# Kernel optimization log

Measured on AMD Instinct MI355X. Metric: run time of the kernel, lower is better.

Reference implementation:

```python
import jax, jax.numpy as jnp
import numpy as np
from jax import lax

N_VNS = 65536
N_CNS = 32768
DV = 4                      # VN degree per graph
N_EDGES = N_VNS * DV
BATCH = 64
NUM_ITER = 8
LLR_MAX = 20.0
ATANH_CLIP = 1.0 - 1e-7


def _graph(rng, n_vns, n_cns, dv):
    # edges sorted by VN (matches argsort(vn_con) in the original)
    vn = np.repeat(np.arange(n_vns, dtype=np.int32), dv)
    cn = rng.integers(0, n_cns, size=n_vns * dv).astype(np.int32)
    perm_v2c = np.argsort(cn, kind='stable').astype(np.int32)   # ind_cn
    perm_c2v = np.argsort(perm_v2c, kind='stable').astype(np.int32)  # ind_cn_inv
    return vn, cn, perm_v2c, perm_c2v


def setup_inputs() -> dict:
    rng = np.random.default_rng(0)
    vn_x, cn_x, pv_x, pc_x = _graph(rng, N_VNS, N_CNS, DV)
    vn_z, cn_z, pv_z, pc_z = _graph(rng, N_VNS, N_CNS, DV)
    key = jax.random.key(0)
    k1, k2, k3 = jax.random.split(key, 3)
    # channel LLRs for X/Y/Z errors (positive-ish, typical for low error rate)
    llr_ch = jax.random.uniform(k1, (3, N_VNS, BATCH), jnp.float32) * 10.0
    syndrome_x = jax.random.randint(k2, (N_CNS, BATCH), 0, 2, jnp.int32)
    syndrome_z = jax.random.randint(k3, (N_CNS, BATCH), 0, 2, jnp.int32)
    return {
        'llr_ch': llr_ch,
        'syndrome_x': syndrome_x,
        'syndrome_z': syndrome_z,
        'vn_ids_x': jnp.asarray(vn_x),
        'vn_ids_z': jnp.asarray(vn_z),
        'cn_ids_x': jnp.asarray(cn_x[pv_x]),   # CN id per edge, in CN-sorted order
        'cn_ids_z': jnp.asarray(cn_z[pv_z]),
        'perm_v2c_x': jnp.asarray(pv_x),
        'perm_v2c_z': jnp.asarray(pv_z),
        'perm_c2v_x': jnp.asarray(pc_x),
        'perm_c2v_z': jnp.asarray(pc_z),
        'num_iter': NUM_ITER,
    }


def _vn_update(msg_x, msg_z, llrx, llry, llrz, vn_x, vn_z, n_vns):
    # per-VN sums of incoming c2v messages (msg_* are [E, B], VN-sorted)
    sum_x = jax.ops.segment_sum(msg_x, vn_x, num_segments=n_vns)  # from H_x graph
    sum_z = jax.ops.segment_sum(msg_z, vn_z, num_segments=n_vns)  # from H_z graph
    llry_all = sum_x + sum_z + llry
    llrx_hx = sum_z + llrx
    llrz_hz = sum_x + llrz
    # extrinsic per-edge LLRs (exclude intrinsic message)
    llrz_hx = llrz_hz[vn_x] - msg_x
    llry_hx = llry_all[vn_x] - msg_x
    llrx_hz = llrx_hx[vn_z] - msg_z
    llry_hz = llry_all[vn_z] - msg_z
    # quaternary -> binary marginalization: log((1+e^-a)/(e^-b + e^-c))
    new_msg_x = jax.nn.softplus(-llrx_hx)[vn_x] - jnp.logaddexp(-llrz_hx, -llry_hx)
    new_msg_z = jax.nn.softplus(-llrz_hz)[vn_z] - jnp.logaddexp(-llrx_hz, -llry_hz)
    return new_msg_x, new_msg_z


def _cn_update_tanh(msg, cn_ids, n_cns, synd_pm):
    # msg: [E, B] in CN-sorted order; synd_pm: [C, B] in {+1,-1}
    t = jnp.tanh(msg * 0.5)
    t = jnp.where(t == 0.0, 1e-12, t)
    prod = jax.ops.segment_prod(t, cn_ids, num_segments=n_cns)  # [C, B]
    prod = prod * synd_pm
    ext = prod[cn_ids] / t                      # extrinsic product
    ext = jnp.where(jnp.abs(ext) < 1e-7, 0.0, ext)
    ext = jnp.clip(ext, -ATANH_CLIP, ATANH_CLIP)
    return 2.0 * jnp.arctanh(ext)


def reference(llr_ch, syndrome_x, syndrome_z, vn_ids_x, vn_ids_z,
              cn_ids_x, cn_ids_z, perm_v2c_x, perm_v2c_z,
              perm_c2v_x, perm_c2v_z, num_iter):
    n_vns = llr_ch.shape[1]
    n_cns_x = syndrome_x.shape[0]
    n_cns_z = syndrome_z.shape[0]
    batch = llr_ch.shape[2]
    ex = vn_ids_x.shape[0]
    ez = vn_ids_z.shape[0]
    dt = llr_ch.dtype

    llr = jnp.clip(llr_ch, -LLR_MAX, LLR_MAX)
    llrx, llry, llrz = llr[0], llr[1], llr[2]
    sx = (1.0 - 2.0 * syndrome_x).astype(dt)  # {0,1} -> {+1,-1}
    sz = (1.0 - 2.0 * syndrome_z).astype(dt)

    def step(carry, _):
        msg_x, msg_z = carry
        nmx, nmz = _vn_update(msg_x, msg_z, llrx, llry, llrz,
                              vn_ids_x, vn_ids_z, n_vns)
        nmx = jnp.clip(nmx, -LLR_MAX, LLR_MAX)
        nmz = jnp.clip(nmz, -LLR_MAX, LLR_MAX)
        # permute VN-order -> CN-order, CN update, permute back
        cx = _cn_update_tanh(nmx[perm_v2c_x], cn_ids_x, n_cns_x, sx)
        cz = _cn_update_tanh(nmz[perm_v2c_z], cn_ids_z, n_cns_z, sz)
        return (cx[perm_c2v_x], cz[perm_c2v_z]), None

    init = (jnp.zeros((ex, batch), dt), jnp.zeros((ez, batch), dt))
    (msg_x, msg_z), _ = lax.scan(step, init, None, length=num_iter)

    # final marginals (sum_only VN update)
    sum_x = jax.ops.segment_sum(msg_x, vn_ids_x, num_segments=n_vns)
    sum_z = jax.ops.segment_sum(msg_z, vn_ids_z, num_segments=n_vns)
    llrx_hx = sum_z + llrx
    llry_all = sum_x + sum_z + llry
    llrz_hz = sum_x + llrz
    return jnp.stack([llrx_hx, llry_all, llrz_hz])  # [3, N, B]
```

## Files before the change

### kernel.cpp

```cpp
#include <hip/hip_runtime.h>

#define N_VNS 65536
#define N_CNS 32768
#define DV 4
#define NE (N_VNS * DV)
#define B 64
#define BH 16
#define NQ (B / BH)
#define NITER 8

#define TANH10 0.9999999958776927

__device__ __forceinline__ double sp_(double y) {
    return fmax(y, 0.0) + log1p(exp(-fabs(y)));
}
__device__ __forceinline__ double clipllr(double x) {
    return fmin(fmax(x, -20.0), 20.0);
}

__global__ void rowptr_k(const int* __restrict__ cn_x, const int* __restrict__ cn_z,
                         int* __restrict__ sx, int* __restrict__ ex,
                         int* __restrict__ sz, int* __restrict__ ez) {
    int i = blockIdx.x * blockDim.x + threadIdx.x;
    const int* cn = blockIdx.y ? cn_z : cn_x;
    int* s = blockIdx.y ? sz : sx;
    int* e = blockIdx.y ? ez : ex;
    int c = cn[i];
    if (i == 0 || cn[i - 1] != c) s[c] = i;
    if (i == NE - 1 || cn[i + 1] != c) e[c] = i + 1;
}

template <bool FIRST>
__global__ void vn_k(const float* __restrict__ llr,
                     const double* __restrict__ mLx, const double* __restrict__ mLz,
                     double* __restrict__ tx, double* __restrict__ tz,
                     int q) {
    int tid = blockIdx.x * blockDim.x + threadIdx.x;
    int v = tid >> 4, b = tid & 15;
    long base = (long)v * (DV * BH) + b;

    double mx[DV], mz[DV], exk[DV], ezk[DV];
    double sumx = 0.0, sumz = 0.0;
#pragma unroll
    for (int k = 0; k < DV; ++k) {
        if (FIRST) { mx[k] = 0.0; mz[k] = 0.0; exk[k] = 0.0; ezk[k] = 0.0; }
        else {
            mx[k] = mLx[base + k * BH];  exk[k] = tx[base + k * BH];
            mz[k] = mLz[base + k * BH];  ezk[k] = tz[base + k * BH];
        }
        sumx += mx[k]; sumz += mz[k];
    }
    long li = (long)v * B + q * BH + b;
    double lx = clipllr((double)llr[li]);
    double ly = clipllr((double)llr[(long)N_VNS * B + li]);
    double lz = clipllr((double)llr[2L * N_VNS * B + li]);

    double llrx_hx  = sumz + lx;
    double llry_all = sumx + sumz + ly;
    double llrz_hz  = sumx + lz;

    double dX = fabs(llrz_hz - llry_all);
    double cX = sp_(-llrx_hx) + fmin(llrz_hz, llry_all) - log1p(exp(-dX));
    double tCX = tanh(0.5 * cX);
    double dZ = fabs(llrx_hx - llry_all);
    double cZ = sp_(-llrz_hz) + fmin(llrx_hx, llry_all) - log1p(exp(-dZ));
    double tCZ = tanh(0.5 * cZ);

#pragma unroll
    for (int k = 0; k < DV; ++k) {
        double tn = (tCX - exk[k]) / (1.0 - tCX * exk[k]);
        tn = fmin(fmax(tn, -TANH10), TANH10);
        if (tn == 0.0) tn = 1e-12;
        tx[base + k * BH] = tn;

        double tm = (tCZ - ezk[k]) / (1.0 - tCZ * ezk[k]);
        tm = fmin(fmax(tm, -TANH10), TANH10);
        if (tm == 0.0) tm = 1e-12;
        tz[base + k * BH] = tm;
    }
}

__global__ void cn_k(const int* __restrict__ synd_x, const int* __restrict__ synd_z,
                     const int* __restrict__ pv_x, const int* __restrict__ pv_z,
                     const int* __restrict__ sx, const int* __restrict__ ex_,
                     const int* __restrict__ sz, const int* __restrict__ ez_,
                     double* __restrict__ mLx, double* __restrict__ mLz,
                     double* __restrict__ tx, double* __restrict__ tz,
                     int q) {
    const double ACLIP = 1.0 - 1e-7;
    int wid = threadIdx.x >> 4;
    int c = blockIdx.x * 16 + wid;
    int b = threadIdx.x & 15;
    bool gz = (blockIdx.y != 0);
    const int* pv   = gz ? pv_z : pv_x;
    const int* synd = gz ? synd_z : synd_x;
    double* t       = gz ? tz : tx;
    double* mL      = gz ? mLz : mLx;
    int s = (gz ? sz : sx)[c];
    int e = (gz ? ez_ : ex_)[c];

    double prod = 1.0 - 2.0 * (double)synd[c * B + q * BH + b];
    for (int i = s; i < e; ++i) {
        prod *= t[(long)pv[i] * BH + b];
    }
    for (int i = s; i < e; ++i) {
        long r = (long)pv[i] * BH + b;
        double tv = t[r];
        double e2 = prod / tv;
        e2 = (fabs(e2) < 1e-7) ? 0.0 : e2;
        e2 = fmin(fmax(e2, -ACLIP), ACLIP);
        t[r]  = e2;
        mL[r] = 2.0 * atanh(e2);
    }
}

__global__ void final_k(const float* __restrict__ llr,
                        const double* __restrict__ mLx,
                        const double* __restrict__ mLz,
                        float* __restrict__ out, int q) {
    int tid = blockIdx.x * blockDim.x + threadIdx.x;
    int v = tid >> 4, b = tid & 15;
    long base = (long)v * (DV * BH) + b;
    double sumx = 0.0, sumz = 0.0;
#pragma unroll
    for (int k = 0; k < DV; ++k) {
        sumx += mLx[base + k * BH];
        sumz += mLz[base + k * BH];
    }
    long li = (long)v * B + q * BH + b;
    double lx = clipllr((double)llr[li]);
    double ly = clipllr((double)llr[(long)N_VNS * B + li]);
    double lz = clipllr((double)llr[2L * N_VNS * B + li]);
    out[li]                   = (float)(sumz + lx);
    out[(long)N_VNS * B + li] = (float)(sumx + sumz + ly);
    out[2L * N_VNS * B + li]  = (float)(sumx + lz);
}

extern "C" void kernel_launch(void* const* d_in, const int* in_sizes, int n_in,
                              void* d_out, int out_size, void* d_ws, size_t ws_size,
                              hipStream_t stream) {
    const float* llr  = (const float*)d_in[0];
    const int* synd_x = (const int*)d_in[1];
    const int* synd_z = (const int*)d_in[2];
    const int* cn_x = (const int*)d_in[5];
    const int* cn_z = (const int*)d_in[6];
    const int* pv_x = (const int*)d_in[7];
    const int* pv_z = (const int*)d_in[8];

    double* mLx = (double*)d_ws;
    double* mLz = mLx + (size_t)NE * BH;
    double* tx  = mLz + (size_t)NE * BH;
    double* tz  = tx  + (size_t)NE * BH;
    int* sx = (int*)(tz + (size_t)NE * BH);
    int* ex = sx + N_CNS;
    int* sz = ex + N_CNS;
    int* ez = sz + N_CNS;

    hipMemsetAsync(sx, 0, 4 * (size_t)N_CNS * sizeof(int), stream);
    rowptr_k<<<dim3(NE / 256, 2), 256, 0, stream>>>(cn_x, cn_z, sx, ex, sz, ez);

    dim3 vn_grid(N_VNS * BH / 256);
    dim3 cn_grid(N_CNS / 16, 2);

    for (int q = 0; q < NQ; ++q) {
        vn_k<true><<<vn_grid, 256, 0, stream>>>(llr, mLx, mLz, tx, tz, q);
        cn_k<<<cn_grid, 256, 0, stream>>>(synd_x, synd_z, pv_x, pv_z,
                                          sx, ex, sz, ez, mLx, mLz, tx, tz, q);
        for (int it = 1; it < NITER; ++it) {
            vn_k<false><<<vn_grid, 256, 0, stream>>>(llr, mLx, mLz, tx, tz, q);
            cn_k<<<cn_grid, 256, 0, stream>>>(synd_x, synd_z, pv_x, pv_z,
                                              sx, ex, sz, ez, mLx, mLz, tx, tz, q);
        }
        final_k<<<vn_grid, 256, 0, stream>>>(llr, mLx, mLz, (float*)d_out, q);
    }
}
```

Before: 4.139 ms.

## Drop stored LLR message arrays, recompute atanh from tanh values, widen batch chunk

The separate per-edge LLR message buffers (mLx/mLz) are removed. The CN kernel now writes only tanh-domain messages, and the VN and final kernels recompute 2*atanh(t) when summing. The batch chunk width goes from 16 to 32 columns, which halves the number of outer passes and kernel launches and gives each CN gather a wider contiguous row. This trades global-memory traffic and workspace for more transcendental FP64 work in the VN kernel. Recomputing atanh on values already clipped to ACLIP should give nearly the same results.

```diff
diff --git a/kernel.cpp b/kernel.cpp
--- a/kernel.cpp
+++ b/kernel.cpp
@@ -5,7 +5,7 @@
 #define DV 4
 #define NE (N_VNS * DV)
 #define B 64
-#define BH 16
+#define BH 32
 #define NQ (B / BH)
 #define NITER 8
 
@@ -32,23 +32,23 @@
 
 template <bool FIRST>
 __global__ void vn_k(const float* __restrict__ llr,
-                     const double* __restrict__ mLx, const double* __restrict__ mLz,
                      double* __restrict__ tx, double* __restrict__ tz,
                      int q) {
     int tid = blockIdx.x * blockDim.x + threadIdx.x;
-    int v = tid >> 4, b = tid & 15;
+    int v = tid >> 5, b = tid & 31;
     long base = (long)v * (DV * BH) + b;
 
-    double mx[DV], mz[DV], exk[DV], ezk[DV];
+    double exk[DV], ezk[DV];
     double sumx = 0.0, sumz = 0.0;
 #pragma unroll
     for (int k = 0; k < DV; ++k) {
-        if (FIRST) { mx[k] = 0.0; mz[k] = 0.0; exk[k] = 0.0; ezk[k] = 0.0; }
+        if (FIRST) { exk[k] = 0.0; ezk[k] = 0.0; }
         else {
-            mx[k] = mLx[base + k * BH];  exk[k] = tx[base + k * BH];
-            mz[k] = mLz[base + k * BH];  ezk[k] = tz[base + k * BH];
+            exk[k] = tx[base + k * BH];
+            ezk[k] = tz[base + k * BH];
+            sumx += 2.0 * atanh(exk[k]);
+            sumz += 2.0 * atanh(ezk[k]);
         }
-        sumx += mx[k]; sumz += mz[k];
     }
     long li = (long)v * B + q * BH + b;
     double lx = clipllr((double)llr[li]);
@@ -84,18 +84,16 @@
                      const int* __restrict__ pv_x, const int* __restrict__ pv_z,
                      const int* __restrict__ sx, const int* __restrict__ ex_,
                      const int* __restrict__ sz, const int* __restrict__ ez_,
-                     double* __restrict__ mLx, double* __restrict__ mLz,
                      double* __restrict__ tx, double* __restrict__ tz,
                      int q) {
     const double ACLIP = 1.0 - 1e-7;
-    int wid = threadIdx.x >> 4;
-    int c = blockIdx.x * 16 + wid;
-    int b = threadIdx.x & 15;
+    int wid = threadIdx.x >> 5;
+    int c = blockIdx.x * 8 + wid;
+    int b = threadIdx.x & 31;
     bool gz = (blockIdx.y != 0);
     const int* pv   = gz ? pv_z : pv_x;
     const int* synd = gz ? synd_z : synd_x;
     double* t       = gz ? tz : tx;
-    double* mL      = gz ? mLz : mLx;
     int s = (gz ? sz : sx)[c];
     int e = (gz ? ez_ : ex_)[c];
 
@@ -109,23 +107,22 @@
         double e2 = prod / tv;
         e2 = (fabs(e2) < 1e-7) ? 0.0 : e2;
         e2 = fmin(fmax(e2, -ACLIP), ACLIP);
-        t[r]  = e2;
-        mL[r] = 2.0 * atanh(e2);
+        t[r] = e2;
     }
 }
 
 __global__ void final_k(const float* __restrict__ llr,
-                        const double* __restrict__ mLx,
-                        const double* __restrict__ mLz,
+                        const double* __restrict__ tx,
+                        const double* __restrict__ tz,
                         float* __restrict__ out, int q) {
     int tid = blockIdx.x * blockDim.x + threadIdx.x;
-    int v = tid >> 4, b = tid & 15;
+    int v = tid >> 5, b = tid & 31;
     long base = (long)v * (DV * BH) + b;
     double sumx = 0.0, sumz = 0.0;
 #pragma unroll
     for (int k = 0; k < DV; ++k) {
-        sumx += mLx[base + k * BH];
-        sumz += mLz[base + k * BH];
+        sumx += 2.0 * atanh(tx[base + k * BH]);
+        sumz += 2.0 * atanh(tz[base + k * BH]);
     }
     long li = (long)v * B + q * BH + b;
     double lx = clipllr((double)llr[li]);
@@ -147,10 +144,8 @@
     const int* pv_x = (const int*)d_in[7];
     const int* pv_z = (const int*)d_in[8];
 
-    double* mLx = (double*)d_ws;
-    double* mLz = mLx + (size_t)NE * BH;
-    double* tx  = mLz + (size_t)NE * BH;
-    double* tz  = tx  + (size_t)NE * BH;
+    double* tx = (double*)d_ws;
+    double* tz = tx + (size_t)NE * BH;
     int* sx = (int*)(tz + (size_t)NE * BH);
     int* ex = sx + N_CNS;
     int* sz = ex + N_CNS;
@@ -160,17 +155,17 @@
     rowptr_k<<<dim3(NE / 256, 2), 256, 0, stream>>>(cn_x, cn_z, sx, ex, sz, ez);
 
     dim3 vn_grid(N_VNS * BH / 256);
-    dim3 cn_grid(N_CNS / 16, 2);
+    dim3 cn_grid(N_CNS / 8, 2);
 
     for (int q = 0; q < NQ; ++q) {
-        vn_k<true><<<vn_grid, 256, 0, stream>>>(llr, mLx, mLz, tx, tz, q);
+        vn_k<true><<<vn_grid, 256, 0, stream>>>(llr, tx, tz, q);
         cn_k<<<cn_grid, 256, 0, stream>>>(synd_x, synd_z, pv_x, pv_z,
-                                          sx, ex, sz, ez, mLx, mLz, tx, tz, q);
+                                          sx, ex, sz, ez, tx, tz, q);
         for (int it = 1; it < NITER; ++it) {
-            vn_k<false><<<vn_grid, 256, 0, stream>>>(llr, mLx, mLz, tx, tz, q);
+            vn_k<false><<<vn_grid, 256, 0, stream>>>(llr, tx, tz, q);
             cn_k<<<cn_grid, 256, 0, stream>>>(synd_x, synd_z, pv_x, pv_z,
-                                              sx, ex, sz, ez, mLx, mLz, tx, tz, q);
+                                              sx, ex, sz, ez, tx, tz, q);
         }
-        final_k<<<vn_grid, 256, 0, stream>>>(llr, mLx, mLz, (float*)d_out, q);
+        final_k<<<vn_grid, 256, 0, stream>>>(llr, tx, tz, (float*)d_out, q);
     }
 }
```

Result: faster. 3.467 ms (-16.2%).
